# Kernel tuning notes

Hardware: AMD Instinct MI355X
Metric: run time of the kernel (lower is better)

The kernel has to match this reference:

```python
import jax, jax.numpy as jnp
import numpy as np

WS, OWS, NHEAD = 4, 6, 6          # window, overlap window = 4 + int(0.5*4), heads
B, CIN, COU, H, W = 2, 192, 192, 224, 224
MID = CIN  # r = 1


def calc_rpi_oca(ws=WS, ows=OWS):
    # relative position index between ws x ws query window and ows x ows overlapping kv window
    co = np.stack(np.meshgrid(np.arange(ws), np.arange(ws), indexing='ij')).reshape(2, -1)
    ce = np.stack(np.meshgrid(np.arange(ows), np.arange(ows), indexing='ij')).reshape(2, -1)
    rel = (ce[:, None, :] - co[:, :, None]).transpose(1, 2, 0) + (ws - 1)  # [ws*ws, ows*ows, 2], >= 0
    idx = rel[..., 0] * (ws + ows - 1) + rel[..., 1]                       # in [0, (ws+ows-1)^2)
    return jnp.asarray(idx)  # [16, 36]

RPI = calc_rpi_oca()


def conv2d(x, w, b, pad):
    out = jax.lax.conv_general_dilated(x, w, (1, 1), [(pad, pad), (pad, pad)],
                                       dimension_numbers=('NCHW', 'OIHW', 'NCHW'))
    return out + b[None, :, None, None]


def group_norm(x, g, b, groups, eps=1e-5):
    n = x.shape[0]
    xg = x.reshape(n, groups, -1)
    mu = xg.mean(-1, keepdims=True)
    var = xg.var(-1, keepdims=True)
    xn = ((xg - mu) * jax.lax.rsqrt(var + eps)).reshape(x.shape)
    return xn * g[None, :, None, None] + b[None, :, None, None]


def layer_norm(x, g, b, eps=1e-5):
    mu = x.mean(-1, keepdims=True)
    var = x.var(-1, keepdims=True)
    return (x - mu) * jax.lax.rsqrt(var + eps) * g + b


def ocab(x, h, w, ln1_g, ln1_b, qkv_w, qkv_b, rpb, proj_w, proj_b,
         ln2_g, ln2_b, fc1_w, fc1_b, fc2_w, fc2_b):
    b, _, c = x.shape
    nh, nw, d = h // WS, w // WS, c // NHEAD
    shortcut = x
    xn = layer_norm(x, ln1_g, ln1_b).reshape(b, h, w, c)
    qkv = xn @ qkv_w + qkv_b                                  # [b,h,w,3c] laid out [q|k|v]
    q = qkv[..., :c]
    kv = jnp.stack([qkv[..., c:2 * c], qkv[..., 2 * c:]])     # [2,b,h,w,c]
    # non-overlapping query windows -> [b*nwin, 16, NHEAD, d]
    qw = q.reshape(b, nh, WS, nw, WS, c).transpose(0, 1, 3, 2, 4, 5).reshape(b * nh * nw, WS * WS, NHEAD, d)
    # overlapping kv windows = Unfold(kernel=OWS, stride=WS, pad=(OWS-WS)//2)
    pad = (OWS - WS) // 2
    kvp = jnp.pad(kv, ((0, 0), (0, 0), (pad, pad), (pad, pad), (0, 0)))
    rows = (jnp.arange(nh) * WS)[:, None] + jnp.arange(OWS)[None, :]   # [nh, OWS]
    cols = (jnp.arange(nw) * WS)[:, None] + jnp.arange(OWS)[None, :]   # [nw, OWS]
    patches = kvp[:, :, rows[:, None, :, None], cols[None, :, None, :], :]  # [2,b,nh,nw,OWS,OWS,c]
    kvw = patches.reshape(2, b * nh * nw, OWS * OWS, NHEAD, d)
    kw, vw = kvw[0], kvw[1]
    attn = jnp.einsum('wqhd,wkhd->whqk', qw * (d ** -0.5), kw)  # [b*nwin, NHEAD, 16, 36]
    bias = rpb[RPI.reshape(-1)].reshape(WS * WS, OWS * OWS, NHEAD).transpose(2, 0, 1)
    attn = jax.nn.softmax(attn + bias[None], axis=-1)
    out = jnp.einsum('whqk,wkhd->wqhd', attn, vw).reshape(b, nh, nw, WS, WS, c)
    out = out.transpose(0, 1, 3, 2, 4, 5).reshape(b, h * w, c)  # window_reverse
    out = out @ proj_w + proj_b + shortcut
    xm = layer_norm(out, ln2_g, ln2_b)
    mlp = jax.nn.gelu(xm @ fc1_w + fc1_b, approximate=False) @ fc2_w + fc2_b
    return out + mlp


def atoca_forward(x, conv1_w, conv1_b, gn1_g, gn1_b, conv2_w, conv2_b, gn2_g, gn2_b,
                  conv3_w, conv3_b, ln1_g, ln1_b, qkv_w, qkv_b, rpb, proj_w, proj_b,
                  ln2_g, ln2_b, fc1_w, fc1_b, fc2_w, fc2_b):
    Bx, C, Hx, Wx = x.shape
    shortcut = x
    # raw row-major reshape, exactly as the torch code (not a spatial window partition)
    out = x.reshape(Bx * (Hx // WS) * (Wx // WS), C, WS, WS)
    out = conv2d(out, conv1_w, conv1_b, 1)
    out = jax.nn.silu(group_norm(out, gn1_g, gn1_b, NHEAD))
    out = out.transpose(0, 2, 3, 1).reshape(Bx, Hx * Wx, -1)
    out = ocab(out, Hx, Wx, ln1_g, ln1_b, qkv_w, qkv_b, rpb, proj_w, proj_b,
               ln2_g, ln2_b, fc1_w, fc1_b, fc2_w, fc2_b)
    out = out.reshape(Bx * (Hx // WS) * (Wx // WS), WS, WS, -1).transpose(0, 3, 1, 2)
    out = conv2d(out, conv2_w, conv2_b, 1)
    out = group_norm(out, gn2_g, gn2_b, NHEAD)
    out = out.reshape(Bx, -1, Hx, Wx)
    out = out + conv2d(shortcut, conv3_w, conv3_b, 0)
    return jax.nn.relu(out)


def setup_inputs() -> dict:
    key = jax.random.key(0)
    ks = iter(jax.random.split(key, 32))
    rn = lambda shape, s=0.02: (s * jax.random.normal(next(ks), shape)).astype(jnp.float32)
    return {
        'x': jax.random.normal(next(ks), (B, CIN, H, W), dtype=jnp.float32),
        'conv1_w': rn((MID, CIN, 3, 3)), 'conv1_b': rn((MID,)),
        'gn1_g': jnp.ones((MID,), jnp.float32), 'gn1_b': jnp.zeros((MID,), jnp.float32),
        'conv2_w': rn((COU, MID, 3, 3)), 'conv2_b': rn((COU,)),
        'gn2_g': jnp.ones((COU,), jnp.float32), 'gn2_b': jnp.zeros((COU,), jnp.float32),
        'conv3_w': rn((COU, CIN, 1, 1)), 'conv3_b': rn((COU,)),
        'ln1_g': jnp.ones((MID,), jnp.float32), 'ln1_b': jnp.zeros((MID,), jnp.float32),
        'qkv_w': rn((MID, 3 * MID)), 'qkv_b': rn((3 * MID,)),
        'rpb': rn(((WS + OWS - 1) ** 2, NHEAD)),
        'proj_w': rn((MID, MID)), 'proj_b': rn((MID,)),
        'ln2_g': jnp.ones((MID,), jnp.float32), 'ln2_b': jnp.zeros((MID,), jnp.float32),
        'fc1_w': rn((MID, 2 * MID)), 'fc1_b': rn((2 * MID,)),
        'fc2_w': rn((2 * MID, MID)), 'fc2_b': rn((MID,)),
    }


def reference(x, conv1_w, conv1_b, gn1_g, gn1_b, conv2_w, conv2_b, gn2_g, gn2_b,
              conv3_w, conv3_b, ln1_g, ln1_b, qkv_w, qkv_b, rpb, proj_w, proj_b,
              ln2_g, ln2_b, fc1_w, fc1_b, fc2_w, fc2_b):
    return atoca_forward(x, conv1_w, conv1_b, gn1_g, gn1_b, conv2_w, conv2_b, gn2_g, gn2_b,
                         conv3_w, conv3_b, ln1_g, ln1_b, qkv_w, qkv_b, rpb, proj_w, proj_b,
                         ln2_g, ln2_b, fc1_w, fc1_b, fc2_w, fc2_b)
```

## Files before the change

kernel.cpp:

```cpp
#include <hip/hip_runtime.h>
#include <hip/hip_bf16.h>
#include <math.h>

typedef __hip_bfloat16 bf16;
typedef __attribute__((ext_vector_type(8))) short s8v;
typedef __attribute__((ext_vector_type(4))) short s4v;
typedef __attribute__((ext_vector_type(4))) float f32x4;
typedef __attribute__((ext_vector_type(2))) _Float16 h2;

constexpr int CB   = 2;
constexpr int CH   = 224, CW = 224;
constexpr int NHW  = 56;
constexpr int NPATCH = CB * NHW * NHW;
constexpr int TOKPB  = CH * CW;
constexpr int MTOK   = CB * TOKPB;
constexpr size_t SECSZ = 19267584;

constexpr size_t B_T0  = 0;
constexpr size_t B_P2  = B_T0 + 38535168;
constexpr size_t B_P3  = B_P2 + 115605504;
constexpr size_t B_P4  = B_P3 + 38535168;
constexpr size_t B_WF1 = B_P4 + 38535168;
constexpr size_t B_WF2 = B_WF1 + 1327104;
constexpr size_t B_W3F = B_WF2 + 1327104;
constexpr size_t B_WQ  = B_W3F + 147456;
constexpr size_t B_WP  = B_WQ + 221184;
constexpr size_t B_WG1 = B_WP + 73728;
constexpr size_t B_WG2 = B_WG1 + 147456;
constexpr size_t WS_NEEDED = B_WG2 + 147456;

__device__ __forceinline__ float ldf(const float* p) { return *p; }
__device__ __forceinline__ float ldf(const bf16* p)  { return __bfloat162float(*p); }
__device__ __forceinline__ void  stf(float* p, float v) { *p = v; }
__device__ __forceinline__ void  stf(bf16* p, float v)  { *p = __float2bfloat16(v); }
__device__ __forceinline__ unsigned short f2bf(float f) {
    unsigned u = __builtin_bit_cast(unsigned, f);
    unsigned r = (u + 0x7fffu + ((u >> 16) & 1u)) >> 16;
    return (unsigned short)r;
}
__device__ __forceinline__ float bf2f(short s) {
    unsigned u = ((unsigned)(unsigned short)s) << 16;
    return __builtin_bit_cast(float, u);
}

__global__ void build_wf_kernel(const float* __restrict__ w, short* __restrict__ wf) {
    int o = blockIdx.x * 256 + threadIdx.x;
    if (o >= 331776) return;
    int within = o & 511, frag = o >> 9;
    int l = within >> 3, j = within & 7;
    int nt = frag % 12, t2 = frag / 12, ks = t2 % 6, tap = t2 / 6;
    int co = nt * 16 + (l & 15);
    int ci = ks * 32 + (l >> 4) * 8 + j;
    wf[o] = (short)f2bf(w[(co * 192 + ci) * 9 + tap]);
}
__global__ void build_wgemm_kernel(const float* __restrict__ w, short* __restrict__ wf,
                                   int K, int N) {
    int o = blockIdx.x * 256 + threadIdx.x;
    if (o >= K * N) return;
    int j = o & 7, l = (o >> 3) & 63, f = o >> 9;
    int ntiles = N >> 4;
    int kt = f / ntiles, nt = f % ntiles;
    int k = kt * 32 + (l >> 4) * 8 + j;
    int col = nt * 16 + (l & 15);
    wf[o] = (short)f2bf(w[(size_t)k * N + col]);
}
__global__ void build_w3f_kernel(const float* __restrict__ w, short* __restrict__ wf) {
    int o = blockIdx.x * 256 + threadIdx.x;
    if (o >= 36864) return;
    int j = o & 7, l = (o >> 3) & 63, f = o >> 9;
    int kt = f / 12, ct = f % 12;
    int co = ct * 16 + (l & 15);
    int ci = kt * 32 + (l >> 4) * 8 + j;
    wf[o] = (short)f2bf(w[co * 192 + ci]);
}

template <bool FIRST>
__global__ __launch_bounds__(256, 4) void conv_mfma_kernel(
    const void* __restrict__ srcv, const short* __restrict__ wf,
    const float* __restrict__ bias, const float* __restrict__ gng,
    const float* __restrict__ gnb, bf16* __restrict__ dst)
{
    __shared__ short xs[13056];
    __shared__ float gsum[4][6], gsum2[4][6], gmu[4][6], grs[4][6];
    const int tid  = threadIdx.x;
    const int lane = tid & 63, wid = tid >> 6;
    const int n0   = blockIdx.x * 4;

    if (tid < 24) { gsum[tid / 6][tid % 6] = 0.f; gsum2[tid / 6][tid % 6] = 0.f; }
    for (int u = tid; u < 4 * 192; u += 256) {
        int q = u / 192;
        xs[q * 3264 + 3072 + (u % 192)] = 0;
    }

    if constexpr (FIRST) {
        const float4* sp = (const float4*)((const float*)srcv + (size_t)n0 * 3072);
        #pragma unroll
        for (int u = 0; u < 12; ++u) {
            int idx = u * 256 + tid;
            float4 v = sp[idx];
            int q = idx / 768;
            int li = (idx % 768) * 4;
            int ci = li >> 4, p0 = li & 15;
            float vv[4] = { v.x, v.y, v.z, v.w };
            #pragma unroll
            for (int k = 0; k < 4; ++k) {
                int row = p0 + k;
                int ba = q * 6528 + ((row * 384 + ci * 2) ^ ((row & 7) << 4));
                *(short*)((char*)xs + ba) = (short)f2bf(vv[k]);
            }
        }
    } else {
        const s8v* sp8 = (const s8v*)((const bf16*)srcv + (size_t)n0 * 3072);
        #pragma unroll
        for (int u = 0; u < 6; ++u) {
            int li = u * 256 + tid;
            int r = li / 24, ch = li % 24;
            int q = r >> 4, rl = r & 15;
            s8v val = sp8[li];
            int ba = q * 6528 + ((rl * 384 + ch * 16) ^ ((rl & 7) << 4));
            *(s8v*)((char*)xs + ba) = val;
        }
    }
    __syncthreads();

    const int ntb = wid * 3;
    const int cl  = lane & 15;
    const int kg  = lane >> 4;
    f32x4 acc[3][4];
    #pragma unroll
    for (int t = 0; t < 3; ++t) {
        float bv = bias[(ntb + t) * 16 + cl];
        #pragma unroll
        for (int q = 0; q < 4; ++q) acc[t][q] = (f32x4){ bv, bv, bv, bv };
    }

    const int pi = cl >> 2, pj = cl & 3;
    const s8v* wf8 = (const s8v*)wf;

    for (int tap = 0; tap < 9; ++tap) {
        const int di = tap / 3, dj = tap % 3;
        const int ii = pi + di - 1, jj = pj + dj - 1;
        const bool valid = (ii >= 0 && ii < 4 && jj >= 0 && jj < 4);
        const int nr  = valid ? (ii * 4 + jj) : 16;
        const int rb  = nr * 384;
        const int swz = (nr & 7) << 4;
        #pragma unroll
        for (int ks = 0; ks < 6; ++ks) {
            const s8v* bp = wf8 + (size_t)((tap * 6 + ks) * 12) * 64 + lane;
            s8v b0 = bp[(ntb + 0) * 64];
            s8v b1 = bp[(ntb + 1) * 64];
            s8v b2 = bp[(ntb + 2) * 64];
            const int inner = (rb + ks * 64 + kg * 16) ^ swz;
            #pragma unroll
            for (int q = 0; q < 4; ++q) {
                s8v a = *(const s8v*)((const char*)xs + q * 6528 + inner);
                acc[0][q] = __builtin_amdgcn_mfma_f32_16x16x32_bf16(a, b0, acc[0][q], 0, 0, 0);
                acc[1][q] = __builtin_amdgcn_mfma_f32_16x16x32_bf16(a, b1, acc[1][q], 0, 0, 0);
                acc[2][q] = __builtin_amdgcn_mfma_f32_16x16x32_bf16(a, b2, acc[2][q], 0, 0, 0);
            }
        }
    }

    #pragma unroll
    for (int t = 0; t < 3; ++t) {
        const int g = (ntb + t) >> 1;
        #pragma unroll
        for (int q = 0; q < 4; ++q) {
            f32x4 A = acc[t][q];
            float s  = A[0] + A[1] + A[2] + A[3];
            float s2 = A[0]*A[0] + A[1]*A[1] + A[2]*A[2] + A[3]*A[3];
            #pragma unroll
            for (int off = 32; off; off >>= 1) { s += __shfl_xor(s, off); s2 += __shfl_xor(s2, off); }
            if (lane == 0) { atomicAdd(&gsum[q][g], s); atomicAdd(&gsum2[q][g], s2); }
        }
    }
    __syncthreads();
    if (tid < 24) {
        int q = tid / 6, g = tid % 6;
        float mu  = gsum[q][g] * (1.f / 512.f);
        float var = gsum2[q][g] * (1.f / 512.f) - mu * mu;
        gmu[q][g] = mu; grs[q][g] = rsqrtf(var + 1e-5f);
    }
    __syncthreads();

    if constexpr (FIRST) {
        #pragma unroll
        for (int t = 0; t < 3; ++t) {
            const int co = (ntb + t) * 16 + cl, g = (ntb + t) >> 1;
            const float gg = gng[co], gb = gnb[co];
            #pragma unroll
            for (int q = 0; q < 4; ++q) {
                const float mu = gmu[q][g], rs = grs[q][g];
                bf16* op = dst + (((size_t)(n0 + q) * 16) + kg * 4) * 192 + co;
                #pragma unroll
                for (int r = 0; r < 4; ++r) {
                    float v = (acc[t][q][r] - mu) * rs * gg + gb;
                    v = v / (1.f + expf(-v));
                    op[(size_t)r * 192] = __float2bfloat16(v);
                }
            }
        }
    } else {
        #pragma unroll
        for (int t = 0; t < 3; ++t) {
            const int co = (ntb + t) * 16 + cl, g = (ntb + t) >> 1;
            const float gg = gng[co], gb = gnb[co];
            #pragma unroll
            for (int q = 0; q < 4; ++q) {
                const float mu = gmu[q][g], rs = grs[q][g];
                #pragma unroll
                for (int r = 0; r < 4; ++r) {
                    float v = (acc[t][q][r] - mu) * rs * gg + gb;
                    xs[q * 3072 + co * 16 + kg * 4 + r] = (short)f2bf(v);
                }
            }
        }
        __syncthreads();
        s4v* dp = (s4v*)(dst + (size_t)n0 * 3072);
        const s4v* sps = (const s4v*)xs;
        #pragma unroll
        for (int u = 0; u < 12; ++u) {
            dp[u * 256 + tid] = sps[u * 256 + tid];
        }
    }
}

template <typename TO, bool RES, bool GELU_ACT, bool LN, bool QKVOUT>
__global__ __launch_bounds__(256) void gemm_mfma_kernel(
    const bf16* __restrict__ A, const short* __restrict__ wfb,
    const float* __restrict__ bias, const bf16* __restrict__ res,
    TO* __restrict__ out, int K, int N,
    const float* __restrict__ lng, const float* __restrict__ lnb)
{
    const int tid = threadIdx.x, lane = tid & 63, wid = tid >> 6;
    const int m0 = blockIdx.x * 128, n0 = blockIdx.y * 64;
    const int cl = lane & 15, kg = lane >> 4;
    const int ntiles = N >> 4, nt0 = n0 >> 4;

    f32x4 acc[2][4];
    #pragma unroll
    for (int nf = 0; nf < 4; ++nf) {
        float bv = bias[n0 + nf * 16 + cl];
        acc[0][nf] = (f32x4){ bv, bv, bv, bv };
        acc[1][nf] = (f32x4){ bv, bv, bv, bv };
    }

    const s8v* wf8 = (const s8v*)wfb;

    if constexpr (LN) {
        s8v af[2][6];
        const int r0 = m0 + wid * 32 + cl;
        #pragma unroll
        for (int kt = 0; kt < 6; ++kt) {
            af[0][kt] = *(const s8v*)(A + (size_t)r0 * 192 + kt * 32 + kg * 8);
            af[1][kt] = *(const s8v*)(A + (size_t)(r0 + 16) * 192 + kt * 32 + kg * 8);
        }
        #pragma unroll
        for (int r = 0; r < 2; ++r) {
            float s = 0.f, s2 = 0.f;
            #pragma unroll
            for (int kt = 0; kt < 6; ++kt)
                #pragma unroll
                for (int j = 0; j < 8; ++j) {
                    float v = bf2f(af[r][kt][j]);
                    s += v; s2 += v * v;
                }
            s  += __shfl_xor(s, 16);  s2 += __shfl_xor(s2, 16);
            s  += __shfl_xor(s, 32);  s2 += __shfl_xor(s2, 32);
            const float mu = s * (1.f / 192.f);
            const float rs = rsqrtf(s2 * (1.f / 192.f) - mu * mu + 1e-5f);
            #pragma unroll
            for (int kt = 0; kt < 6; ++kt) {
                const float* gp = lng + kt * 32 + kg * 8;
                const float* bp = lnb + kt * 32 + kg * 8;
                #pragma unroll
                for (int j = 0; j < 8; ++j) {
                    float v = (bf2f(af[r][kt][j]) - mu) * rs * gp[j] + bp[j];
                    af[r][kt][j] = (short)f2bf(v);
                }
            }
        }
        #pragma unroll
        for (int kt = 0; kt < 6; ++kt) {
            #pragma unroll
            for (int nf = 0; nf < 4; ++nf) {
                s8v b = wf8[(size_t)(kt * ntiles + nt0 + nf) * 64 + lane];
                acc[0][nf] = __builtin_amdgcn_mfma_f32_16x16x32_bf16(af[0][kt], b, acc[0][nf], 0, 0, 0);
                acc[1][nf] = __builtin_amdgcn_mfma_f32_16x16x32_bf16(af[1][kt], b, acc[1][nf], 0, 0, 0);
            }
        }
    } else {
        const int nkt = K >> 5;
        for (int kt = 0; kt < nkt; ++kt) {
            s8v a0 = *(const s8v*)(A + (size_t)(m0 + wid * 32 +      cl) * K + kt * 32 + kg * 8);
            s8v a1 = *(const s8v*)(A + (size_t)(m0 + wid * 32 + 16 + cl) * K + kt * 32 + kg * 8);
            #pragma unroll
            for (int nf = 0; nf < 4; ++nf) {
                s8v b = wf8[(size_t)(kt * ntiles + nt0 + nf) * 64 + lane];
                acc[0][nf] = __builtin_amdgcn_mfma_f32_16x16x32_bf16(a0, b, acc[0][nf], 0, 0, 0);
                acc[1][nf] = __builtin_amdgcn_mfma_f32_16x16x32_bf16(a1, b, acc[1][nf], 0, 0, 0);
            }
        }
    }

    #pragma unroll
    for (int rf = 0; rf < 2; ++rf) {
        #pragma unroll
        for (int nf = 0; nf < 4; ++nf) {
            const int col = n0 + nf * 16 + cl;
            #pragma unroll
            for (int r = 0; r < 4; ++r) {
                const int row = m0 + wid * 32 + rf * 16 + kg * 4 + r;
                float v = acc[rf][nf][r];
                if (GELU_ACT) v = 0.5f * v * (1.f + erff(v * 0.70710678118f));
                if (RES) v += ldf(&res[(size_t)row * N + col]);
                if constexpr (QKVOUT) {
                    const int sec = n0 / 192;
                    const int c = col - sec * 192, h = c >> 5, d = c & 31;
                    const int bb2 = row / TOKPB, t = row - bb2 * TOKPB;
                    ((_Float16*)out)[(size_t)sec * SECSZ +
                        ((size_t)(bb2 * 6 + h) * TOKPB + t) * 32 + d] = (_Float16)v;
                } else {
                    stf(&out[(size_t)row * N + col], v);
                }
            }
        }
    }
}

constexpr int HSTR = 1160;
__global__ __launch_bounds__(128) void attn_kernel(
    const _Float16* __restrict__ qf, const float* __restrict__ rpb,
    bf16* __restrict__ out)
{
    __shared__ short kh[6 * HSTR];
    __shared__ short vh[6 * HSTR];
    const int w = blockIdx.x;
    const int b = w / (NHW * NHW), wi = w % (NHW * NHW);
    const int nhi = wi / NHW, nwi = wi % NHW;
    const int tid = threadIdx.x;
    const int r0 = nhi * 4 - 1, c0 = nwi * 4 - 1;
    const _Float16* kfb = qf + SECSZ;
    const _Float16* vfb = qf + 2 * SECSZ;

    #pragma unroll
    for (int it = 0; it < 14; ++it) {
        int v = tid + it * 128;
        if (v < 1728) {
            int kv = v >= 864 ? 1 : 0;
            int u = v - kv * 864;
            int h = u / 144, rem = u % 144, kj = rem >> 2, d0 = (rem & 3) * 8;
            int rr = r0 + kj / 6, cc = c0 + kj % 6;
            s8v val = { 0, 0, 0, 0, 0, 0, 0, 0 };
            if (rr >= 0 && rr < CH && cc >= 0 && cc < CW) {
                const _Float16* src = kv ? vfb : kfb;
                val = *(const s8v*)(src + ((size_t)(b * 6 + h) * TOKPB + rr * CW + cc) * 32 + d0);
            }
            short* dst = kv ? vh : kh;
            *(s8v*)(dst + h * HSTR + kj * 32 + d0) = val;
        }
    }
    __syncthreads();

    if (tid < 96) {
        const int h = tid >> 4, qi = tid & 15;
        const int qr = nhi * 4 + (qi >> 2), qc = nwi * 4 + (qi & 3);
        const _Float16* qp = qf + ((size_t)(b * 6 + h) * TOKPB + qr * CW + qc) * 32;
        h2 qh[16];
        #pragma unroll
        for (int u = 0; u < 4; ++u) {
            uint4 qa = *(const uint4*)(qp + u * 8);
            qh[u * 4 + 0] = __builtin_bit_cast(h2, qa.x);
            qh[u * 4 + 1] = __builtin_bit_cast(h2, qa.y);
            qh[u * 4 + 2] = __builtin_bit_cast(h2, qa.z);
            qh[u * 4 + 3] = __builtin_bit_cast(h2, qa.w);
        }

        float sc[36];
        const short* khb = kh + h * HSTR;
        #pragma unroll
        for (int kj = 0; kj < 36; ++kj) {
            const uint4* kp = (const uint4*)(khb + kj * 32);
            uint4 k0 = kp[0], k1 = kp[1], k2 = kp[2], k3 = kp[3];
            unsigned kwv[16] = { k0.x, k0.y, k0.z, k0.w, k1.x, k1.y, k1.z, k1.w,
                                 k2.x, k2.y, k2.z, k2.w, k3.x, k3.y, k3.z, k3.w };
            float a0 = 0.f, a1 = 0.f, a2 = 0.f, a3 = 0.f;
            #pragma unroll
            for (int e = 0; e < 4; ++e) {
                a0 = __builtin_amdgcn_fdot2(__builtin_bit_cast(h2, kwv[4*e+0]), qh[4*e+0], a0, false);
                a1 = __builtin_amdgcn_fdot2(__builtin_bit_cast(h2, kwv[4*e+1]), qh[4*e+1], a1, false);
                a2 = __builtin_amdgcn_fdot2(__builtin_bit_cast(h2, kwv[4*e+2]), qh[4*e+2], a2, false);
                a3 = __builtin_amdgcn_fdot2(__builtin_bit_cast(h2, kwv[4*e+3]), qh[4*e+3], a3, false);
            }
            const int rel0 = kj / 6 - (qi >> 2) + 3;
            const int rel1 = kj % 6 - (qi & 3) + 3;
            sc[kj] = ((a0 + a1) + (a2 + a3)) * 0.17677669529f + rpb[(rel0 * 9 + rel1) * 6 + h];
        }
        float mx = -1e30f;
        #pragma unroll
        for (int kj = 0; kj < 36; ++kj) mx = fmaxf(mx, sc[kj]);
        float sum = 0.f;
        #pragma unroll
        for (int kj = 0; kj < 36; ++kj) { sc[kj] = __expf(sc[kj] - mx); sum += sc[kj]; }
        const float inv = 1.f / sum;

        h2 o2[16];
        #pragma unroll
        for (int e = 0; e < 16; ++e) o2[e] = (h2){ (_Float16)0.f, (_Float16)0.f };
        const short* vhb = vh + h * HSTR;
        #pragma unroll
        for (int kj = 0; kj < 36; ++kj) {
            const uint4* vp = (const uint4*)(vhb + kj * 32);
            uint4 v0 = vp[0], v1 = vp[1], v2 = vp[2], v3 = vp[3];
            unsigned vwv[16] = { v0.x, v0.y, v0.z, v0.w, v1.x, v1.y, v1.z, v1.w,
                                 v2.x, v2.y, v2.z, v2.w, v3.x, v3.y, v3.z, v3.w };
            const _Float16 ph = (_Float16)sc[kj];
            const h2 ph2 = { ph, ph };
            #pragma unroll
            for (int e = 0; e < 16; ++e)
                o2[e] = __builtin_bit_cast(h2, vwv[e]) * ph2 + o2[e];
        }
        bf16* op = out + ((size_t)(b * TOKPB + qr * CW + qc)) * 192 + h * 32;
        #pragma unroll
        for (int u = 0; u < 8; ++u) {
            s4v pk;
            #pragma unroll
            for (int e = 0; e < 2; ++e) {
                h2 ov = o2[u * 2 + e];
                pk[2 * e]     = (short)f2bf((float)ov[0] * inv);
                pk[2 * e + 1] = (short)f2bf((float)ov[1] * inv);
            }
            *(s4v*)((bf16*)op + u * 4) = pk;
        }
    }
}

__global__ __launch_bounds__(256, 4) void final_mfma_kernel(
    const float* __restrict__ x, const short* __restrict__ w3f,
    const float* __restrict__ b3, const bf16* __restrict__ c2,
    float* __restrict__ out)
{
    __shared__ short xs2[12288];
    const int pix0 = blockIdx.x * 64;
    const int b    = blockIdx.y;
    const int tid = threadIdx.x, lane = tid & 63, wid = tid >> 6;
    const int cl = lane & 15, kg = lane >> 4;
    const float* xb = x + (size_t)b * (192 * TOKPB);

    #pragma unroll
    for (int u = 0; u < 12; ++u) {
        int idx = u * 256 + tid;
        int ci = idx >> 4, p4 = (idx & 15) << 2;
        float4 v = *(const float4*)(xb + (size_t)ci * TOKPB + pix0 + p4);
        float vv[4] = { v.x, v.y, v.z, v.w };
        #pragma unroll
        for (int k = 0; k < 4; ++k) {
            int row = p4 + k;
            int ba = (row * 384 + ci * 2) ^ ((row & 7) << 4);
            *(short*)((char*)xs2 + ba) = (short)f2bf(vv[k]);
        }
    }
    __syncthreads();

    const int ctb = wid * 3;
    f32x4 acc[3][4] = {};
    const s8v* wf8 = (const s8v*)w3f;

    #pragma unroll
    for (int kt = 0; kt < 6; ++kt) {
        s8v a0 = wf8[(size_t)(kt * 12 + ctb + 0) * 64 + lane];
        s8v a1 = wf8[(size_t)(kt * 12 + ctb + 1) * 64 + lane];
        s8v a2 = wf8[(size_t)(kt * 12 + ctb + 2) * 64 + lane];
        #pragma unroll
        for (int pt = 0; pt < 4; ++pt) {
            int row = pt * 16 + cl;
            int ba = (row * 384 + kt * 64 + kg * 16) ^ ((row & 7) << 4);
            s8v bfr = *(const s8v*)((const char*)xs2 + ba);
            acc[0][pt] = __builtin_amdgcn_mfma_f32_16x16x32_bf16(a0, bfr, acc[0][pt], 0, 0, 0);
            acc[1][pt] = __builtin_amdgcn_mfma_f32_16x16x32_bf16(a1, bfr, acc[1][pt], 0, 0, 0);
            acc[2][pt] = __builtin_amdgcn_mfma_f32_16x16x32_bf16(a2, bfr, acc[2][pt], 0, 0, 0);
        }
    }

    #pragma unroll
    for (int t = 0; t < 3; ++t) {
        #pragma unroll
        for (int r = 0; r < 4; ++r) {
            const int co = (ctb + t) * 16 + kg * 4 + r;
            const float bb = b3[co];
            const size_t rowbase = (size_t)b * (192 * TOKPB) + (size_t)co * TOKPB + pix0;
            #pragma unroll
            for (int pt = 0; pt < 4; ++pt) {
                const size_t f = rowbase + pt * 16 + cl;
                float v = acc[t][pt][r] + bb + bf2f(__builtin_bit_cast(short, c2[f]));
                out[f] = fmaxf(v, 0.f);
            }
        }
    }
}

extern "C" void kernel_launch(void* const* d_in, const int* in_sizes, int n_in,
                              void* d_out, int out_size, void* d_ws, size_t ws_size,
                              hipStream_t stream)
{
    if (ws_size < WS_NEEDED) return;

    const float* x       = (const float*)d_in[0];
    const float* conv1_w = (const float*)d_in[1];
    const float* conv1_b = (const float*)d_in[2];
    const float* gn1_g   = (const float*)d_in[3];
    const float* gn1_b   = (const float*)d_in[4];
    const float* conv2_w = (const float*)d_in[5];
    const float* conv2_b = (const float*)d_in[6];
    const float* gn2_g   = (const float*)d_in[7];
    const float* gn2_b   = (const float*)d_in[8];
    const float* conv3_w = (const float*)d_in[9];
    const float* conv3_b = (const float*)d_in[10];
    const float* ln1_g   = (const float*)d_in[11];
    const float* ln1_b   = (const float*)d_in[12];
    const float* qkv_w   = (const float*)d_in[13];
    const float* qkv_b   = (const float*)d_in[14];
    const float* rpb     = (const float*)d_in[15];
    const float* proj_w  = (const float*)d_in[16];
    const float* proj_b  = (const float*)d_in[17];
    const float* ln2_g   = (const float*)d_in[18];
    const float* ln2_b   = (const float*)d_in[19];
    const float* fc1_w   = (const float*)d_in[20];
    const float* fc1_b   = (const float*)d_in[21];
    const float* fc2_w   = (const float*)d_in[22];
    const float* fc2_b   = (const float*)d_in[23];

    char* wsb = (char*)d_ws;
    bf16*  T0  = (bf16*)(wsb + B_T0);
    _Float16* QF = (_Float16*)(wsb + B_P2);
    bf16*  HID = (bf16*)(wsb + B_P2);
    bf16*  P3  = (bf16*)(wsb + B_P3);
    bf16*  P4  = (bf16*)(wsb + B_P4);
    short* WF1 = (short*)(wsb + B_WF1);
    short* WF2 = (short*)(wsb + B_WF2);
    short* W3F = (short*)(wsb + B_W3F);
    short* WQ  = (short*)(wsb + B_WQ);
    short* WP  = (short*)(wsb + B_WP);
    short* WG1 = (short*)(wsb + B_WG1);
    short* WG2 = (short*)(wsb + B_WG2);
    float* OUT = (float*)d_out;

    build_wf_kernel<<<(331776 + 255) / 256, 256, 0, stream>>>(conv1_w, WF1);
    build_wf_kernel<<<(331776 + 255) / 256, 256, 0, stream>>>(conv2_w, WF2);
    build_w3f_kernel<<<(36864 + 255) / 256, 256, 0, stream>>>(conv3_w, W3F);
    build_wgemm_kernel<<<(110592 + 255) / 256, 256, 0, stream>>>(qkv_w, WQ, 192, 576);
    build_wgemm_kernel<<<(36864 + 255) / 256, 256, 0, stream>>>(proj_w, WP, 192, 192);
    build_wgemm_kernel<<<(73728 + 255) / 256, 256, 0, stream>>>(fc1_w, WG1, 192, 384);
    build_wgemm_kernel<<<(73728 + 255) / 256, 256, 0, stream>>>(fc2_w, WG2, 384, 192);

    conv_mfma_kernel<true><<<NPATCH / 4, 256, 0, stream>>>(x, WF1, conv1_b, gn1_g, gn1_b, T0);
    gemm_mfma_kernel<_Float16, false, false, true, true><<<dim3(MTOK / 128, 9), 256, 0, stream>>>(
        T0, WQ, qkv_b, nullptr, QF, 192, 576, ln1_g, ln1_b);
    attn_kernel<<<NPATCH, 128, 0, stream>>>(QF, rpb, P3);
    gemm_mfma_kernel<bf16, true, false, false, false><<<dim3(MTOK / 128, 3), 256, 0, stream>>>(
        P3, WP, proj_b, T0, P4, 192, 192, nullptr, nullptr);
    gemm_mfma_kernel<bf16, false, true, true, false><<<dim3(MTOK / 128, 6), 256, 0, stream>>>(
        P4, WG1, fc1_b, nullptr, HID, 192, 384, ln2_g, ln2_b);
    gemm_mfma_kernel<bf16, true, false, false, false><<<dim3(MTOK / 128, 3), 256, 0, stream>>>(
        HID, WG2, fc2_b, P4, P3, 384, 192, nullptr, nullptr);
    conv_mfma_kernel<false><<<NPATCH / 4, 256, 0, stream>>>(P3, WF2, conv2_b, gn2_g, gn2_b, P4);
    final_mfma_kernel<<<dim3(TOKPB / 64, CB), 256, 0, stream>>>(x, W3F, conv3_b, P4, OUT);
}
```

Before: 606.9 us.

## Load A row-tile once per block and loop over all N tiles in GEMM

The token GEMMs now use a 1D grid over M. Each block loads its 128-row A tile (and LayerNorm-normalizes it) once into registers, then loops over every 64-column N chunk. Before, each N-tile block reloaded A and recomputed LayerNorm. This cuts redundant global reads of activations and repeated LN math, at the cost of fewer blocks, less parallelism and higher register pressure (K=384 keeps 24 s8v A fragments live).

```diff
diff --git a/kernel.cpp b/kernel.cpp
--- a/kernel.cpp
+++ b/kernel.cpp
@@ -225,44 +225,37 @@
     }
 }
 
-template <typename TO, bool RES, bool GELU_ACT, bool LN, bool QKVOUT>
+template <typename TO, bool RES, bool GELU_ACT, bool LN, bool QKVOUT, int NKT>
 __global__ __launch_bounds__(256) void gemm_mfma_kernel(
     const bf16* __restrict__ A, const short* __restrict__ wfb,
     const float* __restrict__ bias, const bf16* __restrict__ res,
-    TO* __restrict__ out, int K, int N,
+    TO* __restrict__ out, int N,
     const float* __restrict__ lng, const float* __restrict__ lnb)
 {
     const int tid = threadIdx.x, lane = tid & 63, wid = tid >> 6;
-    const int m0 = blockIdx.x * 128, n0 = blockIdx.y * 64;
+    const int m0 = blockIdx.x * 128;
     const int cl = lane & 15, kg = lane >> 4;
-    const int ntiles = N >> 4, nt0 = n0 >> 4;
-
-    f32x4 acc[2][4];
-    #pragma unroll
-    for (int nf = 0; nf < 4; ++nf) {
-        float bv = bias[n0 + nf * 16 + cl];
-        acc[0][nf] = (f32x4){ bv, bv, bv, bv };
-        acc[1][nf] = (f32x4){ bv, bv, bv, bv };
-    }
-
-    const s8v* wf8 = (const s8v*)wfb;
-
+    constexpr int K = NKT * 32;
+    const int ntiles = N >> 4;
+
+    s8v af0[NKT], af1[NKT];
+    const int r0 = m0 + wid * 32 + cl;
+    #pragma unroll
+    for (int kt = 0; kt < NKT; ++kt) {
+        af0[kt] = *(const s8v*)(A + (size_t)r0 * K + kt * 32 + kg * 8);
+        af1[kt] = *(const s8v*)(A + (size_t)(r0 + 16) * K + kt * 32 + kg * 8);
+    }
     if constexpr (LN) {
-        s8v af[2][6];
-        const int r0 = m0 + wid * 32 + cl;
-        #pragma unroll
-        for (int kt = 0; kt < 6; ++kt) {
-            af[0][kt] = *(const s8v*)(A + (size_t)r0 * 192 + kt * 32 + kg * 8);
-            af[1][kt] = *(const s8v*)(A + (size_t)(r0 + 16) * 192 + kt * 32 + kg * 8);
-        }
+        static_assert(!LN || NKT == 6, "LN requires K==192");
         #pragma unroll
         for (int r = 0; r < 2; ++r) {
+            s8v* af = r ? af1 : af0;
             float s = 0.f, s2 = 0.f;
             #pragma unroll
-            for (int kt = 0; kt < 6; ++kt)
+            for (int kt = 0; kt < NKT; ++kt)
                 #pragma unroll
                 for (int j = 0; j < 8; ++j) {
-                    float v = bf2f(af[r][kt][j]);
+                    float v = bf2f(af[kt][j]);
                     s += v; s2 += v * v;
                 }
             s  += __shfl_xor(s, 16);  s2 += __shfl_xor(s2, 16);
@@ -270,58 +263,57 @@
             const float mu = s * (1.f / 192.f);
             const float rs = rsqrtf(s2 * (1.f / 192.f) - mu * mu + 1e-5f);
             #pragma unroll
-            for (int kt = 0; kt < 6; ++kt) {
+            for (int kt = 0; kt < NKT; ++kt) {
                 const float* gp = lng + kt * 32 + kg * 8;
                 const float* bp = lnb + kt * 32 + kg * 8;
                 #pragma unroll
                 for (int j = 0; j < 8; ++j) {
-                    float v = (bf2f(af[r][kt][j]) - mu) * rs * gp[j] + bp[j];
-                    af[r][kt][j] = (short)f2bf(v);
+                    float v = (bf2f(af[kt][j]) - mu) * rs * gp[j] + bp[j];
+                    af[kt][j] = (short)f2bf(v);
                 }
             }
         }
-        #pragma unroll
-        for (int kt = 0; kt < 6; ++kt) {
+    }
+
+    const s8v* wf8 = (const s8v*)wfb;
+    for (int nt0 = 0; nt0 < ntiles; nt0 += 4) {
+        const int n0 = nt0 * 16;
+        f32x4 acc[2][4];
+        #pragma unroll
+        for (int nf = 0; nf < 4; ++nf) {
+            float bv = bias[n0 + nf * 16 + cl];
+            acc[0][nf] = (f32x4){ bv, bv, bv, bv };
+            acc[1][nf] = (f32x4){ bv, bv, bv, bv };
+        }
+        #pragma unroll
+        for (int kt = 0; kt < NKT; ++kt) {
             #pragma unroll
             for (int nf = 0; nf < 4; ++nf) {
                 s8v b = wf8[(size_t)(kt * ntiles + nt0 + nf) * 64 + lane];
-                acc[0][nf] = __builtin_amdgcn_mfma_f32_16x16x32_bf16(af[0][kt], b, acc[0][nf], 0, 0, 0);
-                acc[1][nf] = __builtin_amdgcn_mfma_f32_16x16x32_bf16(af[1][kt], b, acc[1][nf], 0, 0, 0);
-            }
-        }
-    } else {
-        const int nkt = K >> 5;
-        for (int kt = 0; kt < nkt; ++kt) {
-            s8v a0 = *(const s8v*)(A + (size_t)(m0 + wid * 32 +      cl) * K + kt * 32 + kg * 8);
-            s8v a1 = *(const s8v*)(A + (size_t)(m0 + wid * 32 + 16 + cl) * K + kt * 32 + kg * 8);
+                acc[0][nf] = __builtin_amdgcn_mfma_f32_16x16x32_bf16(af0[kt], b, acc[0][nf], 0, 0, 0);
+                acc[1][nf] = __builtin_amdgcn_mfma_f32_16x16x32_bf16(af1[kt], b, acc[1][nf], 0, 0, 0);
+            }
+        }
+        #pragma unroll
+        for (int rf = 0; rf < 2; ++rf) {
             #pragma unroll
             for (int nf = 0; nf < 4; ++nf) {
-                s8v b = wf8[(size_t)(kt * ntiles + nt0 + nf) * 64 + lane];
-                acc[0][nf] = __builtin_amdgcn_mfma_f32_16x16x32_bf16(a0, b, acc[0][nf], 0, 0, 0);
-                acc[1][nf] = __builtin_amdgcn_mfma_f32_16x16x32_bf16(a1, b, acc[1][nf], 0, 0, 0);
-            }
-        }
-    }
-
-    #pragma unroll
-    for (int rf = 0; rf < 2; ++rf) {
-        #pragma unroll
-        for (int nf = 0; nf < 4; ++nf) {
-            const int col = n0 + nf * 16 + cl;
-            #pragma unroll
-            for (int r = 0; r < 4; ++r) {
-                const int row = m0 + wid * 32 + rf * 16 + kg * 4 + r;
-                float v = acc[rf][nf][r];
-                if (GELU_ACT) v = 0.5f * v * (1.f + erff(v * 0.70710678118f));
-                if (RES) v += ldf(&res[(size_t)row * N + col]);
-                if constexpr (QKVOUT) {
-                    const int sec = n0 / 192;
-                    const int c = col - sec * 192, h = c >> 5, d = c & 31;
-                    const int bb2 = row / TOKPB, t = row - bb2 * TOKPB;
-                    ((_Float16*)out)[(size_t)sec * SECSZ +
-                        ((size_t)(bb2 * 6 + h) * TOKPB + t) * 32 + d] = (_Float16)v;
-                } else {
-                    stf(&out[(size_t)row * N + col], v);
+                const int col = n0 + nf * 16 + cl;
+                #pragma unroll
+                for (int r = 0; r < 4; ++r) {
+                    const int row = m0 + wid * 32 + rf * 16 + kg * 4 + r;
+                    float v = acc[rf][nf][r];
+                    if (GELU_ACT) v = 0.5f * v * (1.f + erff(v * 0.70710678118f));
+                    if (RES) v += ldf(&res[(size_t)row * N + col]);
+                    if constexpr (QKVOUT) {
+                        const int sec = n0 / 192;
+                        const int c = col - sec * 192, h = c >> 5, d = c & 31;
+                        const int bb2 = row / TOKPB, t = row - bb2 * TOKPB;
+                        ((_Float16*)out)[(size_t)sec * SECSZ +
+                            ((size_t)(bb2 * 6 + h) * TOKPB + t) * 32 + d] = (_Float16)v;
+                    } else {
+                        stf(&out[(size_t)row * N + col], v);
+                    }
                 }
             }
         }
@@ -554,15 +546,15 @@
     build_wgemm_kernel<<<(73728 + 255) / 256, 256, 0, stream>>>(fc2_w, WG2, 384, 192);
 
     conv_mfma_kernel<true><<<NPATCH / 4, 256, 0, stream>>>(x, WF1, conv1_b, gn1_g, gn1_b, T0);
-    gemm_mfma_kernel<_Float16, false, false, true, true><<<dim3(MTOK / 128, 9), 256, 0, stream>>>(
-        T0, WQ, qkv_b, nullptr, QF, 192, 576, ln1_g, ln1_b);
+    gemm_mfma_kernel<_Float16, false, false, true, true, 6><<<MTOK / 128, 256, 0, stream>>>(
+        T0, WQ, qkv_b, nullptr, QF, 576, ln1_g, ln1_b);
     attn_kernel<<<NPATCH, 128, 0, stream>>>(QF, rpb, P3);
-    gemm_mfma_kernel<bf16, true, false, false, false><<<dim3(MTOK / 128, 3), 256, 0, stream>>>(
-        P3, WP, proj_b, T0, P4, 192, 192, nullptr, nullptr);
-    gemm_mfma_kernel<bf16, false, true, true, false><<<dim3(MTOK / 128, 6), 256, 0, stream>>>(
-        P4, WG1, fc1_b, nullptr, HID, 192, 384, ln2_g, ln2_b);
-    gemm_mfma_kernel<bf16, true, false, false, false><<<dim3(MTOK / 128, 3), 256, 0, stream>>>(
-        HID, WG2, fc2_b, P4, P3, 384, 192, nullptr, nullptr);
+    gemm_mfma_kernel<bf16, true, false, false, false, 6><<<MTOK / 128, 256, 0, stream>>>(
+        P3, WP, proj_b, T0, P4, 192, nullptr, nullptr);
+    gemm_mfma_kernel<bf16, false, true, true, false, 6><<<MTOK / 128, 256, 0, stream>>>(
+        P4, WG1, fc1_b, nullptr, HID, 384, ln2_g, ln2_b);
+    gemm_mfma_kernel<bf16, true, false, false, false, 12><<<MTOK / 128, 256, 0, stream>>>(
+        HID, WG2, fc2_b, P4, P3, 192, nullptr, nullptr);
     conv_mfma_kernel<false><<<NPATCH / 4, 256, 0, stream>>>(P3, WF2, conv2_b, gn2_g, gn2_b, P4);
     final_mfma_kernel<<<dim3(TOKPB / 64, CB), 256, 0, stream>>>(x, W3F, conv3_b, P4, OUT);
 }
```

New measurement: 636.7 us. 1.05x slower.
